# Optimization experiments

Measured on AMD Instinct MI355X. Metric: run time of the kernel, lower is better.

The kernel has to match this reference:

```python
import jax, jax.numpy as jnp
import numpy as np

N, F, H, FO = 4096, 512, 4, 128  # nodes, in-feat, heads, out-feat per head
NEG_INF = -1e10
LRELU_ALPHA = 0.2


def setup_inputs() -> dict:
    key = jax.random.key(0)
    k_x, k_a, k_w, k_as, k_an = jax.random.split(key, 5)
    X = jax.random.normal(k_x, (N, F), dtype=jnp.float32)
    A = (jax.random.uniform(k_a, (N, N)) < 0.01).astype(jnp.float32)
    A = jnp.minimum(A + jnp.eye(N, dtype=jnp.float32), 1.0)
    W = jax.random.normal(k_w, (H, F, FO), dtype=jnp.float32) * 0.05       # per-head kernels
    b = jnp.zeros((H, FO), dtype=jnp.float32)                               # per-head biases
    a_self = jax.random.normal(k_as, (H, FO), dtype=jnp.float32) * 0.05    # attn_kernel_self (F_,1) per head
    a_neigh = jax.random.normal(k_an, (H, FO), dtype=jnp.float32) * 0.05   # attn_kernel_neigh (F_,1) per head
    return {"X": X, "A": A, "W": W, "b": b, "a_self": a_self, "a_neigh": a_neigh}


def reference(X, A, W, b, a_self, a_neigh):
    # features[h] = X @ W[h] -> [H, N, FO]
    feats = jnp.einsum('nf,hfo->hno', X, W)
    # Nx1 self / neighbor scores per head -> [H, N]
    e_s = jnp.einsum('hno,ho->hn', feats, a_self)
    e_n = jnp.einsum('hno,ho->hn', feats, a_neigh)
    # broadcast-add to [H, N, N], LeakyReLU(0.2), additive adjacency mask
    logits = e_s[:, :, None] + e_n[:, None, :]
    logits = jnp.where(logits > 0, logits, LRELU_ALPHA * logits)
    logits = logits + NEG_INF * (1.0 - A)[None, :, :]
    attn = jax.nn.softmax(logits, axis=-1)          # [H, N, N]
    out = jnp.einsum('hnm,hmo->hno', attn, feats)   # weighted aggregate
    out = out + b[:, None, :]
    # concat heads: [N, H*FO]
    out = jnp.transpose(out, (1, 0, 2)).reshape(X.shape[0], -1)
    return jax.nn.relu(out)
```

## Files before the change

kernel.cpp:

```cpp
#include <hip/hip_runtime.h>
#include <math.h>

#define NODES 4096
#define FIN   512
#define HEADS 4
#define FOUT  128
#define COLS  512

typedef _Float16 half8 __attribute__((ext_vector_type(8)));
typedef float    floatx4 __attribute__((ext_vector_type(4)));

__global__ __launch_bounds__(256) void convert_w(
    const float* __restrict__ W, _Float16* __restrict__ Wt)
{
    int t = blockIdx.x * 256 + threadIdx.x;
    int o = t & 127;
    int hs = t >> 7;
    int h = hs >> 6, seg = hs & 63;
    half8 v;
    #pragma unroll
    for (int i = 0; i < 8; i++)
        v[i] = (_Float16)W[((size_t)(h * FIN) + seg * 8 + i) * FOUT + o];
    *(half8*)&Wt[(size_t)(h * FOUT + o) * FIN + seg * 8] = v;
}

__global__ __launch_bounds__(256) void gemm_mfma(
    const float* __restrict__ X, const _Float16* __restrict__ Bt,
    float* __restrict__ feats)
{
    __shared__ _Float16 Ah[2][64][40];
    __shared__ _Float16 Bh[2][64][40];
    const int tid = threadIdx.x;
    const int rowBase = blockIdx.y * 64;
    const int colBase = blockIdx.x * 64;
    const int lane = tid & 63, w = tid >> 6;
    const int quad = lane >> 4, lk = quad * 8, lm = lane & 15;
    const int sr = tid >> 2;
    const int sk = (tid & 3) * 8;

    const float*    xp = X  + (size_t)(rowBase + sr) * FIN + sk;
    const _Float16* bp = Bt + (size_t)(colBase + sr) * FIN + sk;

    floatx4 acc[4];
    #pragma unroll
    for (int mi = 0; mi < 4; mi++) acc[mi] = (floatx4)0.f;

    float4 xa = *(const float4*)(xp);
    float4 xb = *(const float4*)(xp + 4);
    half8  rb = *(const half8*)(bp);

    for (int it = 0; it < FIN / 32; ++it) {
        const int cur = it & 1;
        half8 ha;
        ha[0] = (_Float16)xa.x; ha[1] = (_Float16)xa.y;
        ha[2] = (_Float16)xa.z; ha[3] = (_Float16)xa.w;
        ha[4] = (_Float16)xb.x; ha[5] = (_Float16)xb.y;
        ha[6] = (_Float16)xb.z; ha[7] = (_Float16)xb.w;
        *(half8*)&Ah[cur][sr][sk] = ha;
        *(half8*)&Bh[cur][sr][sk] = rb;
        if (it + 1 < FIN / 32) {
            int k0 = (it + 1) * 32;
            xa = *(const float4*)(xp + k0);
            xb = *(const float4*)(xp + k0 + 4);
            rb = *(const half8*)(bp + k0);
        }
        __syncthreads();
        half8 bfrag = *(const half8*)&Bh[cur][w * 16 + lm][lk];
        #pragma unroll
        for (int mi = 0; mi < 4; mi++) {
            half8 afrag = *(const half8*)&Ah[cur][mi * 16 + lm][lk];
            acc[mi] = __builtin_amdgcn_mfma_f32_16x16x32_f16(afrag, bfrag, acc[mi], 0, 0, 0);
        }
    }
    #pragma unroll
    for (int mi = 0; mi < 4; mi++) {
        #pragma unroll
        for (int r = 0; r < 4; r++) {
            int row = rowBase + mi * 16 + quad * 4 + r;
            int col = colBase + w * 16 + lm;
            feats[(size_t)row * COLS + col] = acc[mi][r];
        }
    }
}

__global__ __launch_bounds__(256) void scores(
    const float* __restrict__ feats, const float* __restrict__ a_self,
    const float* __restrict__ a_neigh, float* __restrict__ e_s, float* __restrict__ e_n)
{
    const int n = blockIdx.x * 4 + (threadIdx.x >> 6);
    const int l = threadIdx.x & 63;
    float ps[HEADS], pn[HEADS];
    #pragma unroll
    for (int s = 0; s < HEADS; s++) {
        float2 x  = *(const float2*)(feats + (size_t)n * COLS + s * FOUT + 2 * l);
        float2 as = *(const float2*)(a_self  + s * FOUT + 2 * l);
        float2 an = *(const float2*)(a_neigh + s * FOUT + 2 * l);
        ps[s] = x.x * as.x + x.y * as.y;
        pn[s] = x.x * an.x + x.y * an.y;
    }
    #pragma unroll
    for (int off = 32; off > 0; off >>= 1) {
        #pragma unroll
        for (int s = 0; s < HEADS; s++) {
            ps[s] += __shfl_xor(ps[s], off, 64);
            pn[s] += __shfl_xor(pn[s], off, 64);
        }
    }
    if (l == 0) {
        #pragma unroll
        for (int s = 0; s < HEADS; s++) {
            e_s[s * NODES + n] = ps[s];
            e_n[s * NODES + n] = pn[s];
        }
    }
}

__global__ __launch_bounds__(256) void aggregate(
    const float* __restrict__ A, const float* __restrict__ feats,
    const float* __restrict__ e_s, const float* __restrict__ e_n,
    const float* __restrict__ bias, float* __restrict__ out)
{
    const int i = blockIdx.x;
    const int tid = threadIdx.x;
    __shared__ unsigned short s_idx[NODES];
    __shared__ float s_w[HEADS][512];
    __shared__ int   s_cnt;
    if (tid == 0) s_cnt = 0;
    __syncthreads();

    const float4* Arow = (const float4*)(A + (size_t)i * NODES);
    for (int q = tid; q < NODES / 4; q += 256) {
        float4 a = Arow[q];
        int j = q * 4;
        if (a.x != 0.f) s_idx[atomicAdd(&s_cnt, 1)] = (unsigned short)j;
        if (a.y != 0.f) s_idx[atomicAdd(&s_cnt, 1)] = (unsigned short)(j + 1);
        if (a.z != 0.f) s_idx[atomicAdd(&s_cnt, 1)] = (unsigned short)(j + 2);
        if (a.w != 0.f) s_idx[atomicAdd(&s_cnt, 1)] = (unsigned short)(j + 3);
    }
    __syncthreads();
    const int cnt = s_cnt;

    const int h = tid >> 6, lane = tid & 63;
    const float esi = e_s[h * NODES + i];
    const float* enh = e_n + h * NODES;

    float m = -1e30f;
    for (int k = lane; k < cnt; k += 64) {
        float e = esi + enh[s_idx[k]];
        m = fmaxf(m, e > 0.f ? e : 0.2f * e);
    }
    #pragma unroll
    for (int off = 32; off > 0; off >>= 1) m = fmaxf(m, __shfl_xor(m, off, 64));

    const int ci = 2 * tid;
    float acc0 = 0.f, acc1 = 0.f, d = 0.f;
    for (int base = 0; base < cnt; base += 512) {
        int nc = min(512, cnt - base);
        for (int k = lane; k < nc; k += 64) {
            float e = esi + enh[s_idx[base + k]];
            float l = e > 0.f ? e : 0.2f * e;
            float wgt = __expf(l - m);
            s_w[h][k] = wgt;
            d += wgt;
        }
        for (int k0 = 0; k0 < nc; k0 += 8) {
            int kk = nc - k0;
            int   je[8]; float we[8];
            #pragma unroll
            for (int u = 0; u < 8; u++) {
                bool v = (u < kk);
                je[u] = s_idx[base + (v ? k0 + u : k0)];
                we[u] = v ? s_w[h][k0 + u] : 0.f;
            }
            float2 f[8];
            #pragma unroll
            for (int u = 0; u < 8; u++)
                f[u] = *(const float2*)(feats + (size_t)je[u] * COLS + ci);
            #pragma unroll
            for (int u = 0; u < 8; u++) {
                acc0 = fmaf(we[u], f[u].x, acc0);
                acc1 = fmaf(we[u], f[u].y, acc1);
            }
        }
    }
    #pragma unroll
    for (int off = 32; off > 0; off >>= 1) d += __shfl_xor(d, off, 64);
    const float dinv = 1.f / d;

    float2 b2 = *(const float2*)(bias + h * FOUT + (ci & 127));
    float o0 = acc0 * dinv + b2.x;
    float o1 = acc1 * dinv + b2.y;
    *(float2*)(out + (size_t)i * COLS + ci) = make_float2(fmaxf(o0, 0.f), fmaxf(o1, 0.f));
}

extern "C" void kernel_launch(void* const* d_in, const int* in_sizes, int n_in,
                              void* d_out, int out_size, void* d_ws, size_t ws_size,
                              hipStream_t stream) {
    const float* X       = (const float*)d_in[0];
    const float* A       = (const float*)d_in[1];
    const float* W       = (const float*)d_in[2];
    const float* b       = (const float*)d_in[3];
    const float* a_self  = (const float*)d_in[4];
    const float* a_neigh = (const float*)d_in[5];
    float* out = (float*)d_out;

    float*    feats = (float*)d_ws;
    float*    e_s   = feats + (size_t)NODES * COLS;
    float*    e_n   = e_s + HEADS * NODES;
    _Float16* Wt    = (_Float16*)(e_n + HEADS * NODES);

    convert_w<<<128, 256, 0, stream>>>(W, Wt);
    dim3 gA(COLS / 64, NODES / 64);
    gemm_mfma<<<gA, 256, 0, stream>>>(X, Wt, feats);
    scores<<<NODES / 4, 256, 0, stream>>>(feats, a_self, a_neigh, e_s, e_n);
    aggregate<<<NODES, 256, 0, stream>>>(A, feats, e_s, e_n, b, out);
}
```

Measured before the change: 155.0 us.

## Fuse weight conversion and attention scores into GEMM, store features as fp16

The separate weight-transpose kernel is removed: the GEMM reads fp32 W directly, converts it and transposes it into LDS. The scores kernel is folded into the GEMM epilogue through shuffle reductions and atomicAdd into zeroed e_s/e_n buffers. Features are stored in fp16 to halve gather traffic in the aggregation. The aggregation is reworked so each wave handles a subset of neighbors across all 512 columns with 16-byte loads, and the per-wave partials are reduced in LDS. The adjacency scan now uses 64-bit nontemporal loads and the output uses a nontemporal store. Costs are fewer launches and less memory traffic, traded for fp16 rounding of the features and atomic contention on the scores.

```diff
diff --git a/kernel.cpp b/kernel.cpp
--- a/kernel.cpp
+++ b/kernel.cpp
@@ -7,39 +7,29 @@
 #define FOUT  128
 #define COLS  512
 
-typedef _Float16 half8 __attribute__((ext_vector_type(8)));
+typedef _Float16 half8   __attribute__((ext_vector_type(8)));
 typedef float    floatx4 __attribute__((ext_vector_type(4)));
-
-__global__ __launch_bounds__(256) void convert_w(
-    const float* __restrict__ W, _Float16* __restrict__ Wt)
-{
-    int t = blockIdx.x * 256 + threadIdx.x;
-    int o = t & 127;
-    int hs = t >> 7;
-    int h = hs >> 6, seg = hs & 63;
-    half8 v;
-    #pragma unroll
-    for (int i = 0; i < 8; i++)
-        v[i] = (_Float16)W[((size_t)(h * FIN) + seg * 8 + i) * FOUT + o];
-    *(half8*)&Wt[(size_t)(h * FOUT + o) * FIN + seg * 8] = v;
-}
-
-__global__ __launch_bounds__(256) void gemm_mfma(
-    const float* __restrict__ X, const _Float16* __restrict__ Bt,
-    float* __restrict__ feats)
+typedef float    floatx2 __attribute__((ext_vector_type(2)));
+
+__global__ __launch_bounds__(256) void gemm_scores(
+    const float* __restrict__ X, const float* __restrict__ W,
+    const float* __restrict__ a_self, const float* __restrict__ a_neigh,
+    _Float16* __restrict__ feats_h, float* __restrict__ e_s, float* __restrict__ e_n)
 {
     __shared__ _Float16 Ah[2][64][40];
     __shared__ _Float16 Bh[2][64][40];
     const int tid = threadIdx.x;
     const int rowBase = blockIdx.y * 64;
     const int colBase = blockIdx.x * 64;
+    const int h     = colBase >> 7;
+    const int obase = colBase & 127;
     const int lane = tid & 63, w = tid >> 6;
     const int quad = lane >> 4, lk = quad * 8, lm = lane & 15;
-    const int sr = tid >> 2;
-    const int sk = (tid & 3) * 8;
-
-    const float*    xp = X  + (size_t)(rowBase + sr) * FIN + sk;
-    const _Float16* bp = Bt + (size_t)(colBase + sr) * FIN + sk;
+
+    const int sr = tid >> 2, sk = (tid & 3) * 8;
+    const float* xp = X + (size_t)(rowBase + sr) * FIN + sk;
+    const int o = tid & 63, fg = tid >> 6;
+    const float* wp = W + ((size_t)h * FIN + fg * 8) * FOUT + obase + o;
 
     floatx4 acc[4];
     #pragma unroll
@@ -47,22 +37,27 @@
 
     float4 xa = *(const float4*)(xp);
     float4 xb = *(const float4*)(xp + 4);
-    half8  rb = *(const half8*)(bp);
+    float rw[8];
+    #pragma unroll
+    for (int ii = 0; ii < 8; ii++) rw[ii] = wp[(size_t)ii * FOUT];
 
     for (int it = 0; it < FIN / 32; ++it) {
         const int cur = it & 1;
-        half8 ha;
+        half8 ha, hb;
         ha[0] = (_Float16)xa.x; ha[1] = (_Float16)xa.y;
         ha[2] = (_Float16)xa.z; ha[3] = (_Float16)xa.w;
         ha[4] = (_Float16)xb.x; ha[5] = (_Float16)xb.y;
         ha[6] = (_Float16)xb.z; ha[7] = (_Float16)xb.w;
-        *(half8*)&Ah[cur][sr][sk] = ha;
-        *(half8*)&Bh[cur][sr][sk] = rb;
+        #pragma unroll
+        for (int ii = 0; ii < 8; ii++) hb[ii] = (_Float16)rw[ii];
+        *(half8*)&Ah[cur][sr][sk]     = ha;
+        *(half8*)&Bh[cur][o][fg * 8]  = hb;
         if (it + 1 < FIN / 32) {
             int k0 = (it + 1) * 32;
             xa = *(const float4*)(xp + k0);
             xb = *(const float4*)(xp + k0 + 4);
-            rb = *(const half8*)(bp + k0);
+            #pragma unroll
+            for (int ii = 0; ii < 8; ii++) rw[ii] = wp[(size_t)(k0 + ii) * FOUT];
         }
         __syncthreads();
         half8 bfrag = *(const half8*)&Bh[cur][w * 16 + lm][lk];
@@ -72,77 +67,59 @@
             acc[mi] = __builtin_amdgcn_mfma_f32_16x16x32_f16(afrag, bfrag, acc[mi], 0, 0, 0);
         }
     }
+
+    const int col = colBase + w * 16 + lm;
+    const float as = a_self[col], an = a_neigh[col];
     #pragma unroll
     for (int mi = 0; mi < 4; mi++) {
         #pragma unroll
         for (int r = 0; r < 4; r++) {
             int row = rowBase + mi * 16 + quad * 4 + r;
-            int col = colBase + w * 16 + lm;
-            feats[(size_t)row * COLS + col] = acc[mi][r];
+            float v = acc[mi][r];
+            feats_h[(size_t)row * COLS + col] = (_Float16)v;
+            float vs = v * as, vn = v * an;
+            #pragma unroll
+            for (int off = 1; off < 16; off <<= 1) {
+                vs += __shfl_xor(vs, off, 64);
+                vn += __shfl_xor(vn, off, 64);
+            }
+            if (lm == 0) {
+                atomicAdd(&e_s[h * NODES + row], vs);
+                atomicAdd(&e_n[h * NODES + row], vn);
+            }
         }
     }
 }
 
-__global__ __launch_bounds__(256) void scores(
-    const float* __restrict__ feats, const float* __restrict__ a_self,
-    const float* __restrict__ a_neigh, float* __restrict__ e_s, float* __restrict__ e_n)
-{
-    const int n = blockIdx.x * 4 + (threadIdx.x >> 6);
-    const int l = threadIdx.x & 63;
-    float ps[HEADS], pn[HEADS];
-    #pragma unroll
-    for (int s = 0; s < HEADS; s++) {
-        float2 x  = *(const float2*)(feats + (size_t)n * COLS + s * FOUT + 2 * l);
-        float2 as = *(const float2*)(a_self  + s * FOUT + 2 * l);
-        float2 an = *(const float2*)(a_neigh + s * FOUT + 2 * l);
-        ps[s] = x.x * as.x + x.y * as.y;
-        pn[s] = x.x * an.x + x.y * an.y;
-    }
-    #pragma unroll
-    for (int off = 32; off > 0; off >>= 1) {
-        #pragma unroll
-        for (int s = 0; s < HEADS; s++) {
-            ps[s] += __shfl_xor(ps[s], off, 64);
-            pn[s] += __shfl_xor(pn[s], off, 64);
-        }
-    }
-    if (l == 0) {
-        #pragma unroll
-        for (int s = 0; s < HEADS; s++) {
-            e_s[s * NODES + n] = ps[s];
-            e_n[s * NODES + n] = pn[s];
-        }
-    }
-}
-
 __global__ __launch_bounds__(256) void aggregate(
-    const float* __restrict__ A, const float* __restrict__ feats,
+    const float* __restrict__ A, const _Float16* __restrict__ feats_h,
     const float* __restrict__ e_s, const float* __restrict__ e_n,
     const float* __restrict__ bias, float* __restrict__ out)
 {
     const int i = blockIdx.x;
     const int tid = threadIdx.x;
     __shared__ unsigned short s_idx[NODES];
-    __shared__ float s_w[HEADS][512];
+    __shared__ float s_w[HEADS][520];
+    __shared__ float s_part[HEADS][520];
+    __shared__ float s_dinv[HEADS];
     __shared__ int   s_cnt;
     if (tid == 0) s_cnt = 0;
     __syncthreads();
 
-    const float4* Arow = (const float4*)(A + (size_t)i * NODES);
-    for (int q = tid; q < NODES / 4; q += 256) {
-        float4 a = Arow[q];
-        int j = q * 4;
-        if (a.x != 0.f) s_idx[atomicAdd(&s_cnt, 1)] = (unsigned short)j;
-        if (a.y != 0.f) s_idx[atomicAdd(&s_cnt, 1)] = (unsigned short)(j + 1);
-        if (a.z != 0.f) s_idx[atomicAdd(&s_cnt, 1)] = (unsigned short)(j + 2);
-        if (a.w != 0.f) s_idx[atomicAdd(&s_cnt, 1)] = (unsigned short)(j + 3);
+    const unsigned long long* Arow = (const unsigned long long*)(A + (size_t)i * NODES);
+    for (int q = tid; q < NODES / 2; q += 256) {
+        unsigned long long v = __builtin_nontemporal_load(Arow + q);
+        if (v) {
+            if ((unsigned)v)         s_idx[atomicAdd(&s_cnt, 1)] = (unsigned short)(2 * q);
+            if ((unsigned)(v >> 32)) s_idx[atomicAdd(&s_cnt, 1)] = (unsigned short)(2 * q + 1);
+        }
     }
     __syncthreads();
     const int cnt = s_cnt;
 
-    const int h = tid >> 6, lane = tid & 63;
-    const float esi = e_s[h * NODES + i];
-    const float* enh = e_n + h * NODES;
+    const int wv = tid >> 6, lane = tid & 63;
+    const float esi = e_s[wv * NODES + i];
+    const float* enh = e_n + wv * NODES;
 
     float m = -1e30f;
     for (int k = lane; k < cnt; k += 64) {
@@ -152,45 +129,62 @@
     #pragma unroll
     for (int off = 32; off > 0; off >>= 1) m = fmaxf(m, __shfl_xor(m, off, 64));
 
-    const int ci = 2 * tid;
-    float acc0 = 0.f, acc1 = 0.f, d = 0.f;
+    float d = 0.f;
+    float acc[8];
+    #pragma unroll
+    for (int u = 0; u < 8; u++) acc[u] = 0.f;
+    const int hl = lane >> 4;
+    const _Float16* fcol = feats_h + lane * 8;
+
     for (int base = 0; base < cnt; base += 512) {
         int nc = min(512, cnt - base);
         for (int k = lane; k < nc; k += 64) {
             float e = esi + enh[s_idx[base + k]];
             float l = e > 0.f ? e : 0.2f * e;
             float wgt = __expf(l - m);
-            s_w[h][k] = wgt;
+            s_w[wv][k] = wgt;
             d += wgt;
         }
-        for (int k0 = 0; k0 < nc; k0 += 8) {
-            int kk = nc - k0;
-            int   je[8]; float we[8];
-            #pragma unroll
-            for (int u = 0; u < 8; u++) {
-                bool v = (u < kk);
-                je[u] = s_idx[base + (v ? k0 + u : k0)];
-                we[u] = v ? s_w[h][k0 + u] : 0.f;
+        __syncthreads();
+        for (int k0 = wv; k0 < nc; k0 += 16) {
+            int idx[4]; float wt[4];
+            #pragma unroll
+            for (int u = 0; u < 4; u++) {
+                int k = k0 + u * 4;
+                bool vld = (k < nc);
+                int kc = vld ? k : k0;
+                idx[u] = s_idx[base + kc];
+                wt[u]  = vld ? s_w[hl][kc] : 0.f;
             }
-            float2 f[8];
-            #pragma unroll
-            for (int u = 0; u < 8; u++)
-                f[u] = *(const float2*)(feats + (size_t)je[u] * COLS + ci);
-            #pragma unroll
-            for (int u = 0; u < 8; u++) {
-                acc0 = fmaf(we[u], f[u].x, acc0);
-                acc1 = fmaf(we[u], f[u].y, acc1);
-            }
-        }
+            half8 f[4];
+            #pragma unroll
+            for (int u = 0; u < 4; u++)
+                f[u] = *(const half8*)(fcol + (size_t)idx[u] * COLS);
+            #pragma unroll
+            for (int u = 0; u < 4; u++)
+                #pragma unroll
+                for (int e8 = 0; e8 < 8; e8++)
+                    acc[e8] = fmaf(wt[u], (float)f[u][e8], acc[e8]);
+        }
+        __syncthreads();
     }
     #pragma unroll
     for (int off = 32; off > 0; off >>= 1) d += __shfl_xor(d, off, 64);
-    const float dinv = 1.f / d;
-
-    float2 b2 = *(const float2*)(bias + h * FOUT + (ci & 127));
-    float o0 = acc0 * dinv + b2.x;
-    float o1 = acc1 * dinv + b2.y;
-    *(float2*)(out + (size_t)i * COLS + ci) = make_float2(fmaxf(o0, 0.f), fmaxf(o1, 0.f));
+    if (lane == 0) s_dinv[wv] = 1.f / d;
+
+    *(floatx4*)&s_part[wv][lane * 8]     = *(floatx4*)&acc[0];
+    *(floatx4*)&s_part[wv][lane * 8 + 4] = *(floatx4*)&acc[4];
+    __syncthreads();
+
+    const int c = 2 * tid;
+    const int h = c >> 7;
+    float o0 = s_part[0][c]     + s_part[1][c]     + s_part[2][c]     + s_part[3][c];
+    float o1 = s_part[0][c + 1] + s_part[1][c + 1] + s_part[2][c + 1] + s_part[3][c + 1];
+    const float dinv = s_dinv[h];
+    o0 = fmaxf(o0 * dinv + bias[c],     0.f);
+    o1 = fmaxf(o1 * dinv + bias[c + 1], 0.f);
+    floatx2 res; res[0] = o0; res[1] = o1;
+    __builtin_nontemporal_store(res, (floatx2*)(out + (size_t)i * COLS + c));
 }
 
 extern "C" void kernel_launch(void* const* d_in, const int* in_sizes, int n_in,
@@ -204,14 +198,12 @@
     const float* a_neigh = (const float*)d_in[5];
     float* out = (float*)d_out;
 
-    float*    feats = (float*)d_ws;
-    float*    e_s   = feats + (size_t)NODES * COLS;
-    float*    e_n   = e_s + HEADS * NODES;
-    _Float16* Wt    = (_Float16*)(e_n + HEADS * NODES);
-
-    convert_w<<<128, 256, 0, stream>>>(W, Wt);
+    _Float16* feats_h = (_Float16*)d_ws;
+    float*    e_s     = (float*)(feats_h + (size_t)NODES * COLS);
+    float*    e_n     = e_s + HEADS * NODES;
+
+    hipMemsetAsync(e_s, 0, 2 * HEADS * NODES * sizeof(float), stream);
     dim3 gA(COLS / 64, NODES / 64);
-    gemm_mfma<<<gA, 256, 0, stream>>>(X, Wt, feats);
-    scores<<<NODES / 4, 256, 0, stream>>>(feats, a_self, a_neigh, e_s, e_n);
-    aggregate<<<NODES, 256, 0, stream>>>(A, feats, e_s, e_n, b, out);
+    gemm_scores<<<gA, 256, 0, stream>>>(X, W, a_self, a_neigh, feats_h, e_s, e_n);
+    aggregate<<<NODES, 256, 0, stream>>>(A, feats_h, e_s, e_n, b, out);
 }
```

After: 149.2 us. 3.7% less time.
